# Optimization experiments

Measured on AMD Instinct MI355X. Metric: run time of the kernel, lower is better.

## Reference

```python
import jax, jax.numpy as jnp
import numpy as np

HIDDEN = 2048
INTER = 768
NUM_EXPERTS = 32
TOP_K = 4
NUM_TOKENS = 2048


def setup_inputs() -> dict:
    key = jax.random.key(0)
    ks = jax.random.split(key, 5)
    scale = 0.02
    x = jax.random.normal(ks[0], (NUM_TOKENS, HIDDEN), dtype=jnp.float32)
    w_router = jax.random.normal(ks[1], (HIDDEN, NUM_EXPERTS), dtype=jnp.float32) * scale
    w_gate = jax.random.normal(ks[2], (NUM_EXPERTS, HIDDEN, INTER), dtype=jnp.float32) * scale
    w_up = jax.random.normal(ks[3], (NUM_EXPERTS, HIDDEN, INTER), dtype=jnp.float32) * scale
    w_down = jax.random.normal(ks[4], (NUM_EXPERTS, INTER, HIDDEN), dtype=jnp.float32) * scale
    return {"hidden_states": x, "w_router": w_router, "w_gate": w_gate,
            "w_up": w_up, "w_down": w_down}


def reference(hidden_states, w_router, w_gate, w_up, w_down):
    x = hidden_states  # [T, H]
    T = x.shape[0]
    # Router: softmax over experts (in input dtype), top-k, renormalize.
    router_logits = x @ w_router                      # [T, E]
    routing_weights = jax.nn.softmax(router_logits, axis=-1)
    top_w, top_idx = jax.lax.top_k(routing_weights, TOP_K)  # [T, K]
    top_w = top_w / jnp.sum(top_w, axis=-1, keepdims=True)   # norm_topk_prob
    # Dense combine weights: combine[t, e] = routing weight if expert e selected
    # for token t, else 0.  (top-k indices are unique per token.)
    combine = jnp.zeros((T, NUM_EXPERTS), dtype=x.dtype)
    combine = combine.at[jnp.arange(T)[:, None], top_idx].add(top_w)  # [T, E]

    # Scan over experts: each step computes one expert's SwiGLU MLP on all
    # tokens and accumulates it weighted by its combine weight (tokens with
    # zero weight contribute nothing, matching the gather/scatter original).
    def body(acc, expert):
        wg, wu, wd, cw = expert  # [H,I], [H,I], [I,H], [T]
        h = jax.nn.silu(x @ wg) * (x @ wu)   # [T, I]
        return acc + (h @ wd) * cw[:, None], None

    out, _ = jax.lax.scan(body, jnp.zeros_like(x),
                          (w_gate, w_up, w_down, combine.T))
    return out
```

## Files before the change

### kernel.cpp

```cpp
#include <hip/hip_runtime.h>

#define T_TOK 2048
#define HID   2048
#define INTER 768
#define NE    32
#define NSLOT 8192
#define MAXT  96

typedef short bf16x8 __attribute__((ext_vector_type(8)));
typedef float f32x4  __attribute__((ext_vector_type(4)));

__device__ __forceinline__ unsigned short f2b(float f){
  unsigned u = __builtin_bit_cast(unsigned, f);
  u += 0x7fffu + ((u >> 16) & 1u);
  return (unsigned short)(u >> 16);
}
__device__ __forceinline__ unsigned pk2(float a, float b){
  return (unsigned)f2b(a) | ((unsigned)f2b(b) << 16);
}
__device__ __forceinline__ float b2f(unsigned short u){
  unsigned x = ((unsigned)u) << 16;
  return __builtin_bit_cast(float, x);
}

__device__ __forceinline__ void wgbar(){
  asm volatile("s_waitcnt lgkmcnt(0)" ::: "memory");
  __builtin_amdgcn_s_barrier();
  __builtin_amdgcn_sched_barrier(0);
}

#define XB_OFF    0ul
#define GBUF_OFF  8388608ul
#define TKW_OFF   20971520ul
#define TKI_OFF   21004288ul
#define ROWS_OFF  21037056ul
#define WTS_OFF   21069824ul
#define OFFS_OFF  21102592ul
#define LOGIT_OFF 21102848ul
#define CNT_OFF   21364992ul
#define FILL_OFF  21365120ul
#define TLIST_OFF 21365248ul
#define UBUF_OFF  21365760ul
#define ZERO_OFF  21102848ul
#define ZERO_SZ   (262144ul + 128ul + 128ul)

__global__ void convert_x_kernel(const float* __restrict__ x, ushort* __restrict__ xb){
  int i = (blockIdx.x * 256 + threadIdx.x) * 8;
  float4 a = *(const float4*)(x + i);
  float4 b = *(const float4*)(x + i + 4);
  uint4 o;
  o.x = pk2(a.x, a.y);
  o.y = pk2(a.z, a.w);
  o.z = pk2(b.x, b.y);
  o.w = pk2(b.z, b.w);
  *(uint4*)(xb + i) = o;
}

__global__ void router_gemm(const float* __restrict__ x, const float* __restrict__ wr,
                            float* __restrict__ logits){
  const int tt = blockIdx.x;
  const int kb = blockIdx.y;
  __shared__ float xs[64 * 64];
  __shared__ float wsm[64 * 32];
  const int tid = threadIdx.x;
  const int r = tid >> 5, e = tid & 31;
  float acc[8];
#pragma unroll
  for (int i = 0; i < 8; i++) acc[i] = 0.0f;

  for (int sub = 0; sub < 4; ++sub){
    const int k0 = kb * 256 + sub * 64;
    __syncthreads();
#pragma unroll
    for (int j = 0; j < 4; j++){
      int f4 = tid + j * 256;
      int row = f4 >> 4, c4 = f4 & 15;
      float4 v = *(const float4*)(x + (size_t)(tt * 64 + row) * HID + k0 + c4 * 4);
      *(float4*)(xs + row * 64 + c4 * 4) = v;
    }
#pragma unroll
    for (int j = 0; j < 2; j++){
      int f4 = tid + j * 256;
      int row = f4 >> 3, c4 = f4 & 7;
      float4 v = *(const float4*)(wr + (size_t)(k0 + row) * NE + c4 * 4);
      *(float4*)(wsm + row * NE + c4 * 4) = v;
    }
    __syncthreads();
    for (int kk = 0; kk < 64; kk++){
      float wv = wsm[kk * NE + e];
#pragma unroll
      for (int i = 0; i < 8; i++) acc[i] += xs[(r + i * 8) * 64 + kk] * wv;
    }
  }
#pragma unroll
  for (int i = 0; i < 8; i++)
    atomicAdd(&logits[(size_t)(tt * 64 + r + i * 8) * NE + e], acc[i]);
}

__global__ void topk_kernel(const float* __restrict__ logits, float* __restrict__ topk_w,
                            int* __restrict__ topk_i, int* __restrict__ counts){
  int t = blockIdx.x * blockDim.x + threadIdx.x;
  if (t >= T_TOK) return;
  float l[32];
  const float4* lp = (const float4*)(logits + (size_t)t * NE);
#pragma unroll
  for (int i = 0; i < 8; i++){
    float4 v = lp[i];
    l[i*4+0] = v.x; l[i*4+1] = v.y; l[i*4+2] = v.z; l[i*4+3] = v.w;
  }
  float m = l[0];
#pragma unroll
  for (int i = 1; i < 32; i++) m = fmaxf(m, l[i]);
#pragma unroll
  for (int i = 0; i < 32; i++) l[i] = __expf(l[i] - m);
  float wsel[4]; int isel[4];
#pragma unroll
  for (int k = 0; k < 4; k++){
    float best = l[0]; int bi = 0;
#pragma unroll
    for (int i = 1; i < 32; i++){ if (l[i] > best){ best = l[i]; bi = i; } }
    wsel[k] = best; isel[k] = bi; l[bi] = -1.0f;
  }
  float s4 = wsel[0] + wsel[1] + wsel[2] + wsel[3];
  float inv = 1.0f / s4;
#pragma unroll
  for (int k = 0; k < 4; k++){
    topk_w[t * 4 + k] = wsel[k] * inv;
    topk_i[t * 4 + k] = isel[k];
    atomicAdd(&counts[isel[k]], 1);
  }
}

__global__ void prefix_kernel(const int* __restrict__ counts, int* __restrict__ offsets,
                              int* __restrict__ tlist){
  if (threadIdx.x == 0){
    int a = 0; offsets[0] = 0; int nt_ = 0;
    for (int e = 0; e < NE; e++){
      int c = counts[e];
      for (int m = 0; m * 128 < c && nt_ < MAXT; m++) tlist[nt_++] = e | (m << 16);
      a += c; offsets[e + 1] = a;
    }
    for (; nt_ < MAXT; nt_++) tlist[nt_] = -1;
  }
}

__global__ void scatter_kernel(const int* __restrict__ topk_i, const float* __restrict__ topk_w,
                               const int* __restrict__ offsets, int* __restrict__ fill,
                               int* __restrict__ rows, float* __restrict__ wts){
  int gid = blockIdx.x * 256 + threadIdx.x;
  int t = gid >> 2;
  int e = topk_i[gid];
  int pos = atomicAdd(&fill[e], 1);
  int s = offsets[e] + pos;
  rows[s] = t;
  wts[s] = topk_w[gid];
}

#define NT_GU 64
#define A_USH 5120
#define BUF_USH 15360
__global__ __launch_bounds__(512, 2) void guv_kernel(
    const ushort* __restrict__ xb, const float* __restrict__ wg,
    const float* __restrict__ wu, const int* __restrict__ rows,
    const int* __restrict__ counts, const int* __restrict__ offsets,
    const int* __restrict__ tlist, ushort* __restrict__ gbuf,
    ushort* __restrict__ ubuf)
{
  const int w = tlist[blockIdx.y];
  if (w < 0) return;
  const int e = w & 0xffff, mt = w >> 16;
  const int mat = blockIdx.x & 1, nt = blockIdx.x >> 1;
  const int cnt = counts[e], off = offsets[e];
  const int n0 = nt * 256;

  __shared__ __align__(16) ushort lds[2 * BUF_USH];

  const int tid = threadIdx.x;
  const int lane = tid & 63, wv = tid >> 6;

  const int ar = tid >> 2, ablk = tid & 3;
  const int srow = mt * 128 + ar;
  const int tokA = rows[off + (srow < cnt ? srow : 0)];
  const ushort* agp = xb + (size_t)tokA * HID + ablk * 8;
  const int adst = ar * 40 + ablk * 8;

  const float* wsel = mat ? wu : wg;
  const float* bgp = wsel + (size_t)e * (HID * INTER) + (size_t)(wv * 4) * INTER + n0 + lane;
  const int bdst = A_USH + lane * 40 + wv * 4;

  const int wm = wv >> 2, wn = wv & 3;
  const int fr = lane & 15, ko = lane >> 4;
  int aoff[4], boff[4];
#pragma unroll
  for (int mf = 0; mf < 4; mf++) aoff[mf] = (wm * 64 + mf * 16 + fr) * 40 + ko * 8;
#pragma unroll
  for (int nf = 0; nf < 4; nf++) boff[nf] = A_USH + (wn * 64 + nf * 16 + fr) * 40 + ko * 8;

  f32x4 acc[4][4];
#pragma unroll
  for (int i = 0; i < 4; i++)
#pragma unroll
    for (int j = 0; j < 4; j++) acc[i][j] = (f32x4)(0.0f);

  uint4 a0, a1; uint2 b0[4], b1[4];

  auto loadSet = [&](int k0, uint4 &aa, uint2 *bb){
    aa = *(const uint4*)(agp + k0);
#pragma unroll
    for (int i = 0; i < 4; i++){
      float v0 = bgp[(size_t)(k0 + 0) * INTER + i * 64];
      float v1 = bgp[(size_t)(k0 + 1) * INTER + i * 64];
      float v2 = bgp[(size_t)(k0 + 2) * INTER + i * 64];
      float v3 = bgp[(size_t)(k0 + 3) * INTER + i * 64];
      bb[i].x = pk2(v0, v1); bb[i].y = pk2(v2, v3);
    }
  };
  auto writeSet = [&](int base, const uint4 &aa, const uint2 *bb){
    *(uint4*)(lds + base + adst) = aa;
#pragma unroll
    for (int i = 0; i < 4; i++)
      *(uint2*)(lds + base + bdst + i * 2560) = bb[i];
  };
  auto compute = [&](int base){
    bf16x8 a[4], b[4];
#pragma unroll
    for (int mf = 0; mf < 4; mf++) a[mf] = *(const bf16x8*)(lds + base + aoff[mf]);
#pragma unroll
    for (int nf = 0; nf < 4; nf++) b[nf] = *(const bf16x8*)(lds + base + boff[nf]);
#pragma unroll
    for (int mf = 0; mf < 4; mf++)
#pragma unroll
      for (int nf = 0; nf < 4; nf++)
        acc[mf][nf] = __builtin_amdgcn_mfma_f32_16x16x32_bf16(a[mf], b[nf], acc[mf][nf], 0, 0, 0);
  };

  loadSet(0, a0, b0);
  loadSet(32, a1, b1);
  writeSet(0, a0, b0);
  wgbar();

  for (int t = 0; t < NT_GU; t += 2){
    if (t + 2 < NT_GU) loadSet((t + 2) * 32, a0, b0);
    compute(0);
    writeSet(BUF_USH, a1, b1);
    wgbar();
    if (t + 3 < NT_GU) loadSet((t + 3) * 32, a1, b1);
    compute(BUF_USH);
    if (t + 2 < NT_GU){ writeSet(0, a0, b0); wgbar(); }
  }

  ushort* obuf = mat ? ubuf : gbuf;
#pragma unroll
  for (int mf = 0; mf < 4; mf++)
#pragma unroll
    for (int j = 0; j < 4; j++){
      int rl = wm * 64 + mf * 16 + ko * 4 + j;
      int gr = mt * 128 + rl;
      if (gr < cnt){
        size_t rb = (size_t)(off + gr) * INTER + n0;
#pragma unroll
        for (int nf = 0; nf < 4; nf++)
          obuf[rb + wn * 64 + nf * 16 + fr] = f2b(acc[mf][nf][j]);
      }
    }
}

__global__ void fuse_kernel(ushort* __restrict__ gbuf, const ushort* __restrict__ ubuf,
                            const float* __restrict__ wts){
  const int s = blockIdx.x;
  const int c = threadIdx.x * 4;
  const float wt = wts[s];
  size_t base = (size_t)s * INTER + c;
  uint2 gv = *(const uint2*)(gbuf + base);
  uint2 uv = *(const uint2*)(ubuf + base);
  float h[4];
  {
    float g0 = b2f((unsigned short)gv.x),        u0 = b2f((unsigned short)uv.x);
    float g1 = b2f((unsigned short)(gv.x >> 16)), u1 = b2f((unsigned short)(uv.x >> 16));
    float g2 = b2f((unsigned short)gv.y),        u2 = b2f((unsigned short)uv.y);
    float g3 = b2f((unsigned short)(gv.y >> 16)), u3 = b2f((unsigned short)(uv.y >> 16));
    h[0] = (g0 / (1.0f + __expf(-g0))) * u0 * wt;
    h[1] = (g1 / (1.0f + __expf(-g1))) * u1 * wt;
    h[2] = (g2 / (1.0f + __expf(-g2))) * u2 * wt;
    h[3] = (g3 / (1.0f + __expf(-g3))) * u3 * wt;
  }
  uint2 o; o.x = pk2(h[0], h[1]); o.y = pk2(h[2], h[3]);
  *(uint2*)(gbuf + base) = o;
}

#define NT_DN 24
__global__ __launch_bounds__(512, 2) void down_kernel(
    const ushort* __restrict__ hbuf, const float* __restrict__ wd,
    const int* __restrict__ rows, const int* __restrict__ counts,
    const int* __restrict__ offsets, const int* __restrict__ tlist,
    float* __restrict__ out)
{
  const int w = tlist[blockIdx.y];
  if (w < 0) return;
  const int e = w & 0xffff, mt = w >> 16;
  const int nt = blockIdx.x;
  const int cnt = counts[e], off = offsets[e];
  const int n0 = nt * 256;

  __shared__ __align__(16) ushort lds[2 * BUF_USH];

  const int tid = threadIdx.x;
  const int lane = tid & 63, wv = tid >> 6;

  const int ar = tid >> 2, ablk = tid & 3;
  const int srow = mt * 128 + ar;
  const int slotA = off + (srow < cnt ? srow : 0);
  const ushort* agp = hbuf + (size_t)slotA * INTER + ablk * 8;
  const int adst = ar * 40 + ablk * 8;

  const float* bgp = wd + (size_t)e * (INTER * HID) + (size_t)(wv * 4) * HID + n0 + lane;
  const int bdst = A_USH + lane * 40 + wv * 4;

  const int wm = wv >> 2, wn = wv & 3;
  const int fr = lane & 15, ko = lane >> 4;
  int aoff[4], boff[4];
#pragma unroll
  for (int mf = 0; mf < 4; mf++) aoff[mf] = (wm * 64 + mf * 16 + fr) * 40 + ko * 8;
#pragma unroll
  for (int nf = 0; nf < 4; nf++) boff[nf] = A_USH + (wn * 64 + nf * 16 + fr) * 40 + ko * 8;

  f32x4 acc[4][4];
#pragma unroll
  for (int i = 0; i < 4; i++)
#pragma unroll
    for (int j = 0; j < 4; j++) acc[i][j] = (f32x4)(0.0f);

  uint4 a0, a1; uint2 b0[4], b1[4];

  auto loadSet = [&](int k0, uint4 &aa, uint2 *bb){
    aa = *(const uint4*)(agp + k0);
#pragma unroll
    for (int i = 0; i < 4; i++){
      float v0 = bgp[(size_t)(k0 + 0) * HID + i * 64];
      float v1 = bgp[(size_t)(k0 + 1) * HID + i * 64];
      float v2 = bgp[(size_t)(k0 + 2) * HID + i * 64];
      float v3 = bgp[(size_t)(k0 + 3) * HID + i * 64];
      bb[i].x = pk2(v0, v1); bb[i].y = pk2(v2, v3);
    }
  };
  auto writeSet = [&](int base, const uint4 &aa, const uint2 *bb){
    *(uint4*)(lds + base + adst) = aa;
#pragma unroll
    for (int i = 0; i < 4; i++)
      *(uint2*)(lds + base + bdst + i * 2560) = bb[i];
  };
  auto compute = [&](int base){
    bf16x8 a[4], b[4];
#pragma unroll
    for (int mf = 0; mf < 4; mf++) a[mf] = *(const bf16x8*)(lds + base + aoff[mf]);
#pragma unroll
    for (int nf = 0; nf < 4; nf++) b[nf] = *(const bf16x8*)(lds + base + boff[nf]);
#pragma unroll
    for (int mf = 0; mf < 4; mf++)
#pragma unroll
      for (int nf = 0; nf < 4; nf++)
        acc[mf][nf] = __builtin_amdgcn_mfma_f32_16x16x32_bf16(a[mf], b[nf], acc[mf][nf], 0, 0, 0);
  };

  loadSet(0, a0, b0);
  loadSet(32, a1, b1);
  writeSet(0, a0, b0);
  wgbar();

  for (int t = 0; t < NT_DN; t += 2){
    if (t + 2 < NT_DN) loadSet((t + 2) * 32, a0, b0);
    compute(0);
    writeSet(BUF_USH, a1, b1);
    wgbar();
    if (t + 3 < NT_DN) loadSet((t + 3) * 32, a1, b1);
    compute(BUF_USH);
    if (t + 2 < NT_DN){ writeSet(0, a0, b0); wgbar(); }
  }

#pragma unroll
  for (int mf = 0; mf < 4; mf++)
#pragma unroll
    for (int j = 0; j < 4; j++){
      int rl = wm * 64 + mf * 16 + ko * 4 + j;
      int gr = mt * 128 + rl;
      if (gr < cnt){
        int tok = rows[off + gr];
        float* obase = out + (size_t)tok * HID + n0;
#pragma unroll
        for (int nf = 0; nf < 4; nf++)
          atomicAdd(obase + wn * 64 + nf * 16 + fr, acc[mf][nf][j]);
      }
    }
}

extern "C" void kernel_launch(void* const* d_in, const int* in_sizes, int n_in,
                              void* d_out, int out_size, void* d_ws, size_t ws_size,
                              hipStream_t stream){
  const float* x  = (const float*)d_in[0];
  const float* wr = (const float*)d_in[1];
  const float* wg = (const float*)d_in[2];
  const float* wu = (const float*)d_in[3];
  const float* wd = (const float*)d_in[4];
  float* out = (float*)d_out;
  char* ws = (char*)d_ws;

  ushort* xb     = (ushort*)(ws + XB_OFF);
  ushort* gbuf   = (ushort*)(ws + GBUF_OFF);
  ushort* ubuf   = (ushort*)(ws + UBUF_OFF);
  float*  topkw  = (float*)(ws + TKW_OFF);
  int*    topki  = (int*)(ws + TKI_OFF);
  int*    rows   = (int*)(ws + ROWS_OFF);
  float*  wts    = (float*)(ws + WTS_OFF);
  int*    offs   = (int*)(ws + OFFS_OFF);
  float*  logits = (float*)(ws + LOGIT_OFF);
  int*    counts = (int*)(ws + CNT_OFF);
  int*    fill   = (int*)(ws + FILL_OFF);
  int*    tlist  = (int*)(ws + TLIST_OFF);

  hipMemsetAsync(ws + ZERO_OFF, 0, ZERO_SZ, stream);
  hipMemsetAsync(d_out, 0, (size_t)out_size * sizeof(float), stream);

  convert_x_kernel<<<2048, 256, 0, stream>>>(x, xb);
  router_gemm<<<dim3(32, 8), 256, 0, stream>>>(x, wr, logits);
  topk_kernel<<<8, 256, 0, stream>>>(logits, topkw, topki, counts);
  prefix_kernel<<<1, 64, 0, stream>>>(counts, offs, tlist);
  scatter_kernel<<<32, 256, 0, stream>>>(topki, topkw, offs, fill, rows, wts);
  guv_kernel<<<dim3(6, MAXT), 512, 0, stream>>>(xb, wg, wu, rows, counts, offs, tlist, gbuf, ubuf);
  fuse_kernel<<<NSLOT, 192, 0, stream>>>(gbuf, ubuf, wts);
  down_kernel<<<dim3(8, MAXT), 512, 0, stream>>>(gbuf, wd, rows, counts, offs, tlist, out);
}
```

Before: 374.4 us.

## Vectorize weight loads, shrink guv tiles, and replace atomic scatter with slot buffer combine

Weight tiles are now loaded as float4 rows, coalesced and vectorized, and transposed while being written to LDS, replacing the scalar strided loads. The gate/up kernel moves to 128-wide N tiles with more blocks and higher occupancy bounds, and the down kernel's warp layout changes to 2x8 fragments per warp. When the workspace is large enough, the down projection writes bf16 per-slot outputs and a new combine kernel sums the four slots per token. This replaces the float atomics and the output memset. The cost is an extra 32MB bf16 buffer round trip and added bf16 rounding of the partial outputs.

Measured after the change: 771.6 us. +106.1%, slower.

```diff
diff --git a/kernel.cpp b/kernel.cpp
--- a/kernel.cpp
+++ b/kernel.cpp
@@ -40,7 +40,10 @@
 #define CNT_OFF   21364992ul
 #define FILL_OFF  21365120ul
 #define TLIST_OFF 21365248ul
-#define UBUF_OFF  21365760ul
+#define T2S_OFF   21365760ul
+#define UBUF_OFF  21398528ul
+#define SBUF_OFF  33981440ul
+#define WS_NEED   (SBUF_OFF + 33554432ul)
 #define ZERO_OFF  21102848ul
 #define ZERO_SZ   (262144ul + 128ul + 128ul)
 
@@ -146,7 +149,8 @@
 
 __global__ void scatter_kernel(const int* __restrict__ topk_i, const float* __restrict__ topk_w,
                                const int* __restrict__ offsets, int* __restrict__ fill,
-                               int* __restrict__ rows, float* __restrict__ wts){
+                               int* __restrict__ rows, float* __restrict__ wts,
+                               int* __restrict__ t2s){
   int gid = blockIdx.x * 256 + threadIdx.x;
   int t = gid >> 2;
   int e = topk_i[gid];
@@ -154,12 +158,13 @@
   int s = offsets[e] + pos;
   rows[s] = t;
   wts[s] = topk_w[gid];
-}
-
-#define NT_GU 64
-#define A_USH 5120
-#define BUF_USH 15360
-__global__ __launch_bounds__(512, 2) void guv_kernel(
+  t2s[gid] = s;
+}
+
+#define NTK_GU 64
+#define GA_SZ 5120
+#define GBUF_USH 10240
+__global__ __launch_bounds__(512, 6) void guv_kernel(
     const ushort* __restrict__ xb, const float* __restrict__ wg,
     const float* __restrict__ wu, const int* __restrict__ rows,
     const int* __restrict__ counts, const int* __restrict__ offsets,
@@ -171,90 +176,88 @@
   const int e = w & 0xffff, mt = w >> 16;
   const int mat = blockIdx.x & 1, nt = blockIdx.x >> 1;
   const int cnt = counts[e], off = offsets[e];
-  const int n0 = nt * 256;
-
-  __shared__ __align__(16) ushort lds[2 * BUF_USH];
+  const int n0 = nt * 128;
+
+  __shared__ __align__(16) ushort lds[2 * GBUF_USH];
 
   const int tid = threadIdx.x;
   const int lane = tid & 63, wv = tid >> 6;
 
-  const int ar = tid >> 2, ablk = tid & 3;
+  const int ar = tid >> 2, aq = tid & 3;
   const int srow = mt * 128 + ar;
   const int tokA = rows[off + (srow < cnt ? srow : 0)];
-  const ushort* agp = xb + (size_t)tokA * HID + ablk * 8;
-  const int adst = ar * 40 + ablk * 8;
-
+  const ushort* agp = xb + (size_t)tokA * HID + aq * 8;
+  const int adst = ar * 40 + aq * 8;
+
+  const int q = tid >> 5, cq = tid & 31;
   const float* wsel = mat ? wu : wg;
-  const float* bgp = wsel + (size_t)e * (HID * INTER) + (size_t)(wv * 4) * INTER + n0 + lane;
-  const int bdst = A_USH + lane * 40 + wv * 4;
-
-  const int wm = wv >> 2, wn = wv & 3;
+  const float* bgp = wsel + (size_t)e * (HID * INTER) + (size_t)(2 * q) * INTER + n0 + cq * 4;
+
+  const int wm = wv >> 1, wn = wv & 1;
   const int fr = lane & 15, ko = lane >> 4;
-  int aoff[4], boff[4];
-#pragma unroll
-  for (int mf = 0; mf < 4; mf++) aoff[mf] = (wm * 64 + mf * 16 + fr) * 40 + ko * 8;
-#pragma unroll
-  for (int nf = 0; nf < 4; nf++) boff[nf] = A_USH + (wn * 64 + nf * 16 + fr) * 40 + ko * 8;
-
-  f32x4 acc[4][4];
-#pragma unroll
-  for (int i = 0; i < 4; i++)
+  int aoff[2], boff[4];
+#pragma unroll
+  for (int mf = 0; mf < 2; mf++) aoff[mf] = (wm * 32 + mf * 16 + fr) * 40 + ko * 8;
+#pragma unroll
+  for (int nf = 0; nf < 4; nf++) boff[nf] = GA_SZ + (wn * 64 + nf * 16 + fr) * 40 + ko * 8;
+
+  f32x4 acc[2][4];
+#pragma unroll
+  for (int i = 0; i < 2; i++)
 #pragma unroll
     for (int j = 0; j < 4; j++) acc[i][j] = (f32x4)(0.0f);
 
-  uint4 a0, a1; uint2 b0[4], b1[4];
-
-  auto loadSet = [&](int k0, uint4 &aa, uint2 *bb){
+  uint4 a0, a1;
+  float4 b0r0, b0r1, b1r0, b1r1;
+
+  auto loadSet = [&](int k0, uint4 &aa, float4 &r0, float4 &r1){
     aa = *(const uint4*)(agp + k0);
+    r0 = *(const float4*)(bgp + (size_t)k0 * INTER);
+    r1 = *(const float4*)(bgp + (size_t)k0 * INTER + INTER);
+  };
+  auto writeSet = [&](int base, const uint4 &aa, const float4 &r0, const float4 &r1){
+    *(uint4*)(lds + base + adst) = aa;
+    uint* bd = (uint*)(lds + base + GA_SZ);
 #pragma unroll
     for (int i = 0; i < 4; i++){
-      float v0 = bgp[(size_t)(k0 + 0) * INTER + i * 64];
-      float v1 = bgp[(size_t)(k0 + 1) * INTER + i * 64];
-      float v2 = bgp[(size_t)(k0 + 2) * INTER + i * 64];
-      float v3 = bgp[(size_t)(k0 + 3) * INTER + i * 64];
-      bb[i].x = pk2(v0, v1); bb[i].y = pk2(v2, v3);
-    }
-  };
-  auto writeSet = [&](int base, const uint4 &aa, const uint2 *bb){
-    *(uint4*)(lds + base + adst) = aa;
-#pragma unroll
-    for (int i = 0; i < 4; i++)
-      *(uint2*)(lds + base + bdst + i * 2560) = bb[i];
+      int c = cq * 4 + i;
+      bd[c * 20 + q] = pk2(((const float*)&r0)[i], ((const float*)&r1)[i]);
+    }
   };
   auto compute = [&](int base){
-    bf16x8 a[4], b[4];
-#pragma unroll
-    for (int mf = 0; mf < 4; mf++) a[mf] = *(const bf16x8*)(lds + base + aoff[mf]);
+    bf16x8 a[2], b[4];
+#pragma unroll
+    for (int mf = 0; mf < 2; mf++) a[mf] = *(const bf16x8*)(lds + base + aoff[mf]);
 #pragma unroll
     for (int nf = 0; nf < 4; nf++) b[nf] = *(const bf16x8*)(lds + base + boff[nf]);
 #pragma unroll
-    for (int mf = 0; mf < 4; mf++)
+    for (int mf = 0; mf < 2; mf++)
 #pragma unroll
       for (int nf = 0; nf < 4; nf++)
         acc[mf][nf] = __builtin_amdgcn_mfma_f32_16x16x32_bf16(a[mf], b[nf], acc[mf][nf], 0, 0, 0);
   };
 
-  loadSet(0, a0, b0);
-  loadSet(32, a1, b1);
-  writeSet(0, a0, b0);
+  loadSet(0,  a0, b0r0, b0r1);
+  loadSet(32, a1, b1r0, b1r1);
+  writeSet(0, a0, b0r0, b0r1);
   wgbar();
 
-  for (int t = 0; t < NT_GU; t += 2){
-    if (t + 2 < NT_GU) loadSet((t + 2) * 32, a0, b0);
+  for (int t = 0; t < NTK_GU; t += 2){
+    if (t + 2 < NTK_GU) loadSet((t + 2) * 32, a0, b0r0, b0r1);
     compute(0);
-    writeSet(BUF_USH, a1, b1);
+    writeSet(GBUF_USH, a1, b1r0, b1r1);
     wgbar();
-    if (t + 3 < NT_GU) loadSet((t + 3) * 32, a1, b1);
-    compute(BUF_USH);
-    if (t + 2 < NT_GU){ writeSet(0, a0, b0); wgbar(); }
+    if (t + 3 < NTK_GU) loadSet((t + 3) * 32, a1, b1r0, b1r1);
+    compute(GBUF_USH);
+    if (t + 2 < NTK_GU){ writeSet(0, a0, b0r0, b0r1); wgbar(); }
   }
 
   ushort* obuf = mat ? ubuf : gbuf;
 #pragma unroll
-  for (int mf = 0; mf < 4; mf++)
+  for (int mf = 0; mf < 2; mf++)
 #pragma unroll
     for (int j = 0; j < 4; j++){
-      int rl = wm * 64 + mf * 16 + ko * 4 + j;
+      int rl = wm * 32 + mf * 16 + ko * 4 + j;
       int gr = mt * 128 + rl;
       if (gr < cnt){
         size_t rb = (size_t)(off + gr) * INTER + n0;
@@ -288,12 +291,15 @@
   *(uint2*)(gbuf + base) = o;
 }
 
-#define NT_DN 24
-__global__ __launch_bounds__(512, 2) void down_kernel(
+#define NTK_DN 24
+#define DA_SZ 5120
+#define DBUF_USH 15360
+template<bool SLOT>
+__global__ __launch_bounds__(512, 4) void down_kernel(
     const ushort* __restrict__ hbuf, const float* __restrict__ wd,
     const int* __restrict__ rows, const int* __restrict__ counts,
     const int* __restrict__ offsets, const int* __restrict__ tlist,
-    float* __restrict__ out)
+    float* __restrict__ outp, ushort* __restrict__ sbuf)
 {
   const int w = tlist[blockIdx.y];
   if (w < 0) return;
@@ -302,95 +308,130 @@
   const int cnt = counts[e], off = offsets[e];
   const int n0 = nt * 256;
 
-  __shared__ __align__(16) ushort lds[2 * BUF_USH];
+  __shared__ __align__(16) ushort lds[2 * DBUF_USH];
 
   const int tid = threadIdx.x;
   const int lane = tid & 63, wv = tid >> 6;
 
-  const int ar = tid >> 2, ablk = tid & 3;
+  const int ar = tid >> 2, aq = tid & 3;
   const int srow = mt * 128 + ar;
   const int slotA = off + (srow < cnt ? srow : 0);
-  const ushort* agp = hbuf + (size_t)slotA * INTER + ablk * 8;
-  const int adst = ar * 40 + ablk * 8;
-
-  const float* bgp = wd + (size_t)e * (INTER * HID) + (size_t)(wv * 4) * HID + n0 + lane;
-  const int bdst = A_USH + lane * 40 + wv * 4;
-
-  const int wm = wv >> 2, wn = wv & 3;
+  const ushort* agp = hbuf + (size_t)slotA * INTER + aq * 8;
+  const int adst = ar * 40 + aq * 8;
+
+  const int q = tid >> 5, cq = tid & 31;
+  const float* bgp = wd + (size_t)e * (INTER * HID) + (size_t)(2 * q) * HID + n0 + cq * 4;
+
+  const int wm = wv >> 1, wn = wv & 1;
   const int fr = lane & 15, ko = lane >> 4;
-  int aoff[4], boff[4];
-#pragma unroll
-  for (int mf = 0; mf < 4; mf++) aoff[mf] = (wm * 64 + mf * 16 + fr) * 40 + ko * 8;
-#pragma unroll
-  for (int nf = 0; nf < 4; nf++) boff[nf] = A_USH + (wn * 64 + nf * 16 + fr) * 40 + ko * 8;
-
-  f32x4 acc[4][4];
-#pragma unroll
-  for (int i = 0; i < 4; i++)
-#pragma unroll
-    for (int j = 0; j < 4; j++) acc[i][j] = (f32x4)(0.0f);
-
-  uint4 a0, a1; uint2 b0[4], b1[4];
-
-  auto loadSet = [&](int k0, uint4 &aa, uint2 *bb){
+  int aoff[2], boff[8];
+#pragma unroll
+  for (int mf = 0; mf < 2; mf++) aoff[mf] = (wm * 32 + mf * 16 + fr) * 40 + ko * 8;
+#pragma unroll
+  for (int nf = 0; nf < 8; nf++) boff[nf] = DA_SZ + (wn * 128 + nf * 16 + fr) * 40 + ko * 8;
+
+  f32x4 acc[2][8];
+#pragma unroll
+  for (int i = 0; i < 2; i++)
+#pragma unroll
+    for (int j = 0; j < 8; j++) acc[i][j] = (f32x4)(0.0f);
+
+  uint4 a0, a1;
+  float4 s0[4], s1[4];
+
+  auto loadSet = [&](int k0, uint4 &aa, float4 *bb){
     aa = *(const uint4*)(agp + k0);
+    const float* p = bgp + (size_t)k0 * HID;
+    bb[0] = *(const float4*)(p);
+    bb[1] = *(const float4*)(p + HID);
+    bb[2] = *(const float4*)(p + 128);
+    bb[3] = *(const float4*)(p + HID + 128);
+  };
+  auto writeSet = [&](int base, const uint4 &aa, const float4 *bb){
+    *(uint4*)(lds + base + adst) = aa;
+    uint* bd = (uint*)(lds + base + DA_SZ);
 #pragma unroll
     for (int i = 0; i < 4; i++){
-      float v0 = bgp[(size_t)(k0 + 0) * HID + i * 64];
-      float v1 = bgp[(size_t)(k0 + 1) * HID + i * 64];
-      float v2 = bgp[(size_t)(k0 + 2) * HID + i * 64];
-      float v3 = bgp[(size_t)(k0 + 3) * HID + i * 64];
-      bb[i].x = pk2(v0, v1); bb[i].y = pk2(v2, v3);
-    }
-  };
-  auto writeSet = [&](int base, const uint4 &aa, const uint2 *bb){
-    *(uint4*)(lds + base + adst) = aa;
-#pragma unroll
-    for (int i = 0; i < 4; i++)
-      *(uint2*)(lds + base + bdst + i * 2560) = bb[i];
+      int c = cq * 4 + i;
+      bd[c * 20 + q]         = pk2(((const float*)&bb[0])[i], ((const float*)&bb[1])[i]);
+      bd[(c + 128) * 20 + q] = pk2(((const float*)&bb[2])[i], ((const float*)&bb[3])[i]);
+    }
   };
   auto compute = [&](int base){
-    bf16x8 a[4], b[4];
-#pragma unroll
-    for (int mf = 0; mf < 4; mf++) a[mf] = *(const bf16x8*)(lds + base + aoff[mf]);
-#pragma unroll
-    for (int nf = 0; nf < 4; nf++) b[nf] = *(const bf16x8*)(lds + base + boff[nf]);
-#pragma unroll
-    for (int mf = 0; mf < 4; mf++)
-#pragma unroll
-      for (int nf = 0; nf < 4; nf++)
+    bf16x8 a[2], b[8];
+#pragma unroll
+    for (int mf = 0; mf < 2; mf++) a[mf] = *(const bf16x8*)(lds + base + aoff[mf]);
+#pragma unroll
+    for (int nf = 0; nf < 8; nf++) b[nf] = *(const bf16x8*)(lds + base + boff[nf]);
+#pragma unroll
+    for (int mf = 0; mf < 2; mf++)
+#pragma unroll
+      for (int nf = 0; nf < 8; nf++)
         acc[mf][nf] = __builtin_amdgcn_mfma_f32_16x16x32_bf16(a[mf], b[nf], acc[mf][nf], 0, 0, 0);
   };
 
-  loadSet(0, a0, b0);
-  loadSet(32, a1, b1);
-  writeSet(0, a0, b0);
+  loadSet(0,  a0, s0);
+  loadSet(32, a1, s1);
+  writeSet(0, a0, s0);
   wgbar();
 
-  for (int t = 0; t < NT_DN; t += 2){
-    if (t + 2 < NT_DN) loadSet((t + 2) * 32, a0, b0);
+  for (int t = 0; t < NTK_DN; t += 2){
+    if (t + 2 < NTK_DN) loadSet((t + 2) * 32, a0, s0);
     compute(0);
-    writeSet(BUF_USH, a1, b1);
+    writeSet(DBUF_USH, a1, s1);
     wgbar();
-    if (t + 3 < NT_DN) loadSet((t + 3) * 32, a1, b1);
-    compute(BUF_USH);
-    if (t + 2 < NT_DN){ writeSet(0, a0, b0); wgbar(); }
-  }
-
-#pragma unroll
-  for (int mf = 0; mf < 4; mf++)
+    if (t + 3 < NTK_DN) loadSet((t + 3) * 32, a1, s1);
+    compute(DBUF_USH);
+    if (t + 2 < NTK_DN){ writeSet(0, a0, s0); wgbar(); }
+  }
+
+#pragma unroll
+  for (int mf = 0; mf < 2; mf++)
 #pragma unroll
     for (int j = 0; j < 4; j++){
-      int rl = wm * 64 + mf * 16 + ko * 4 + j;
+      int rl = wm * 32 + mf * 16 + ko * 4 + j;
       int gr = mt * 128 + rl;
       if (gr < cnt){
-        int tok = rows[off + gr];
-        float* obase = out + (size_t)tok * HID + n0;
-#pragma unroll
-        for (int nf = 0; nf < 4; nf++)
-          atomicAdd(obase + wn * 64 + nf * 16 + fr, acc[mf][nf][j]);
+        if (SLOT){
+          ushort* obase = sbuf + (size_t)(off + gr) * HID + n0;
+#pragma unroll
+          for (int nf = 0; nf < 8; nf++)
+            obase[wn * 128 + nf * 16 + fr] = f2b(acc[mf][nf][j]);
+        } else {
+          int tok = rows[off + gr];
+          float* obase = outp + (size_t)tok * HID + n0;
+#pragma unroll
+          for (int nf = 0; nf < 8; nf++)
+            atomicAdd(obase + wn * 128 + nf * 16 + fr, acc[mf][nf][j]);
+        }
       }
     }
+}
+
+__global__ void combine_kernel(const ushort* __restrict__ sbuf, const int* __restrict__ t2s,
+                               float* __restrict__ out){
+  const int t = blockIdx.x;
+  const int c = threadIdx.x * 8;
+  const int s0 = t2s[t * 4 + 0], s1 = t2s[t * 4 + 1];
+  const int s2 = t2s[t * 4 + 2], s3 = t2s[t * 4 + 3];
+  uint4 a = *(const uint4*)(sbuf + (size_t)s0 * HID + c);
+  uint4 b = *(const uint4*)(sbuf + (size_t)s1 * HID + c);
+  uint4 d = *(const uint4*)(sbuf + (size_t)s2 * HID + c);
+  uint4 g = *(const uint4*)(sbuf + (size_t)s3 * HID + c);
+  float r[8];
+#pragma unroll
+  for (int i = 0; i < 4; i++){
+    unsigned ua = ((const unsigned*)&a)[i], ub = ((const unsigned*)&b)[i];
+    unsigned ud = ((const unsigned*)&d)[i], ug = ((const unsigned*)&g)[i];
+    r[2*i]   = b2f((unsigned short)ua) + b2f((unsigned short)ub) +
+               b2f((unsigned short)ud) + b2f((unsigned short)ug);
+    r[2*i+1] = b2f((unsigned short)(ua >> 16)) + b2f((unsigned short)(ub >> 16)) +
+               b2f((unsigned short)(ud >> 16)) + b2f((unsigned short)(ug >> 16));
+  }
+  float4 o0 = { r[0], r[1], r[2], r[3] };
+  float4 o1 = { r[4], r[5], r[6], r[7] };
+  *(float4*)(out + (size_t)t * HID + c)     = o0;
+  *(float4*)(out + (size_t)t * HID + c + 4) = o1;
 }
 
 extern "C" void kernel_launch(void* const* d_in, const int* in_sizes, int n_in,
@@ -407,6 +448,7 @@
   ushort* xb     = (ushort*)(ws + XB_OFF);
   ushort* gbuf   = (ushort*)(ws + GBUF_OFF);
   ushort* ubuf   = (ushort*)(ws + UBUF_OFF);
+  ushort* sbuf   = (ushort*)(ws + SBUF_OFF);
   float*  topkw  = (float*)(ws + TKW_OFF);
   int*    topki  = (int*)(ws + TKI_OFF);
   int*    rows   = (int*)(ws + ROWS_OFF);
@@ -416,16 +458,24 @@
   int*    counts = (int*)(ws + CNT_OFF);
   int*    fill   = (int*)(ws + FILL_OFF);
   int*    tlist  = (int*)(ws + TLIST_OFF);
+  int*    t2s    = (int*)(ws + T2S_OFF);
+
+  const bool slotpath = (ws_size >= WS_NEED);
 
   hipMemsetAsync(ws + ZERO_OFF, 0, ZERO_SZ, stream);
-  hipMemsetAsync(d_out, 0, (size_t)out_size * sizeof(float), stream);
 
   convert_x_kernel<<<2048, 256, 0, stream>>>(x, xb);
   router_gemm<<<dim3(32, 8), 256, 0, stream>>>(x, wr, logits);
   topk_kernel<<<8, 256, 0, stream>>>(logits, topkw, topki, counts);
   prefix_kernel<<<1, 64, 0, stream>>>(counts, offs, tlist);
-  scatter_kernel<<<32, 256, 0, stream>>>(topki, topkw, offs, fill, rows, wts);
-  guv_kernel<<<dim3(6, MAXT), 512, 0, stream>>>(xb, wg, wu, rows, counts, offs, tlist, gbuf, ubuf);
+  scatter_kernel<<<32, 256, 0, stream>>>(topki, topkw, offs, fill, rows, wts, t2s);
+  guv_kernel<<<dim3(12, MAXT), 512, 0, stream>>>(xb, wg, wu, rows, counts, offs, tlist, gbuf, ubuf);
   fuse_kernel<<<NSLOT, 192, 0, stream>>>(gbuf, ubuf, wts);
-  down_kernel<<<dim3(8, MAXT), 512, 0, stream>>>(gbuf, wd, rows, counts, offs, tlist, out);
-}
+  if (slotpath){
+    down_kernel<true><<<dim3(8, MAXT), 512, 0, stream>>>(gbuf, wd, rows, counts, offs, tlist, out, sbuf);
+    combine_kernel<<<T_TOK, 256, 0, stream>>>(sbuf, t2s, out);
+  } else {
+    hipMemsetAsync(d_out, 0, (size_t)out_size * sizeof(float), stream);
+    down_kernel<false><<<dim3(8, MAXT), 512, 0, stream>>>(gbuf, wd, rows, counts, offs, tlist, out, sbuf);
+  }
+}
```
